# Performance work log

Measured on AMD Instinct MI355X. Metric: run time of the kernel, lower is better.

Reference implementation:

```python
import jax, jax.numpy as jnp
import numpy as np

NS, L, H = 8, 2048, 1024
M, E, K = 4096, 8, 2
EPS = 1e-9

def setup_inputs() -> dict:
    key = jax.random.key(0)
    ks = jax.random.split(key, 5)
    s = 0.02
    return {
        "x": jax.random.normal(ks[0], (NS, L, H), jnp.float32),
        "Wr": jax.random.normal(ks[1], (H, E), jnp.float32) * s,
        "br": jnp.zeros((E,), jnp.float32),
        "W1": jax.random.normal(ks[2], (E, H, M), jnp.float32) * s,
        "b1": jnp.zeros((E, M), jnp.float32),
        "W2": jax.random.normal(ks[3], (E, M, H), jnp.float32) * s,
        "b2": jnp.zeros((E, H), jnp.float32),
    }

def reference(x, Wr, br, W1, b1, W2, b2):
    ns, seq, h = x.shape
    flat = x.reshape(-1, h)                      # (N, H); grouping only reshapes, math is per-token
    logits = flat @ Wr + br                      # (N, E)
    probs = jax.nn.softmax(logits, axis=-1)
    vals, idx = jax.lax.top_k(probs, K)          # (N, K)
    w = vals / (jnp.sum(vals, axis=-1, keepdims=True) + EPS)
    out_acc = jnp.zeros_like(flat)
    weight_acc = jnp.zeros((flat.shape[0],), flat.dtype)
    for e in range(E):                           # fixed small expert loop
        we = jnp.sum(w * (idx == e), axis=-1)    # (N,) combine weight for expert e
        hmid = jax.nn.gelu(flat @ W1[e] + b1[e], approximate=False)
        y = hmid @ W2[e] + b2[e]
        out_acc = out_acc + we[:, None] * y
        weight_acc = weight_acc + we
    out = out_acc / (weight_acc[:, None] + EPS)
    return out.reshape(ns, seq, h)
```

## Files before the change

### kernel.cpp

```cpp
#include <hip/hip_runtime.h>
#include <hip/hip_bf16.h>
#include <math.h>

#define NTOK 16384
#define HDIM 1024
#define MDIM 4096
#define NEXP 8
#define EPSV 1e-9f
#define RTOK 32

typedef unsigned short u16;
typedef __attribute__((ext_vector_type(4))) float f32x4;
typedef __attribute__((ext_vector_type(8))) __bf16 bf16x8;
typedef __attribute__((ext_vector_type(8))) unsigned short u16x8;
typedef __attribute__((ext_vector_type(4))) unsigned short u16x4;

#define ASYNC_COPY16(gptr, lptr) \
    __builtin_amdgcn_global_load_lds( \
        (const __attribute__((address_space(1))) void*)(gptr), \
        (__attribute__((address_space(3))) void*)(lptr), 16, 0, 0)

static __device__ __forceinline__ u16 f2bf(float f) {
    unsigned int u = __builtin_bit_cast(unsigned int, f);
    u += 0x7fff + ((u >> 16) & 1);
    return (u16)(u >> 16);
}

static __device__ __forceinline__ float gelu_f(float v) {
    float z2 = -1.5957691216f * v * (1.f + 0.044715f * v * v);
    return v / (1.f + __expf(z2));
}

__global__ __launch_bounds__(256) void router_kernel(
    const float* __restrict__ x, const float* __restrict__ Wr,
    const float* __restrict__ br,
    int* __restrict__ counts, int* __restrict__ ltok, float* __restrict__ lcf,
    u16* __restrict__ xb)
{
    __shared__ int   lcount[NEXP];
    __shared__ int   lbase[NEXP];
    __shared__ int   ltokL[NEXP][RTOK];
    __shared__ float lcfL[NEXP][RTOK];

    int t = threadIdx.x;
    if (t < NEXP) lcount[t] = 0;
    __syncthreads();

    int wave = t >> 6, lane = t & 63;

    for (int it = 0; it < RTOK / 4; ++it) {
        int tok = blockIdx.x * RTOK + it * 4 + wave;
        const float* xr = x + (size_t)tok * HDIM + lane * 16;

        f32x4 xv[4];
        #pragma unroll
        for (int q = 0; q < 4; q++) xv[q] = *reinterpret_cast<const f32x4*>(xr + q * 4);

        u16x8 ob0, ob1;
        #pragma unroll
        for (int j = 0; j < 4; j++) {
            ob0[j]     = f2bf(xv[0][j]);
            ob0[4 + j] = f2bf(xv[1][j]);
            ob1[j]     = f2bf(xv[2][j]);
            ob1[4 + j] = f2bf(xv[3][j]);
        }
        u16* xo = xb + (size_t)tok * HDIM + lane * 16;
        *reinterpret_cast<u16x8*>(xo)     = ob0;
        *reinterpret_cast<u16x8*>(xo + 8) = ob1;

        f32x4 acc0 = {0.f, 0.f, 0.f, 0.f};
        f32x4 acc1 = {0.f, 0.f, 0.f, 0.f};
        #pragma unroll
        for (int q = 0; q < 4; q++) {
            #pragma unroll
            for (int j = 0; j < 4; j++) {
                int h = lane * 16 + q * 4 + j;
                const float* wrow = Wr + (size_t)h * NEXP;
                f32x4 w0 = *reinterpret_cast<const f32x4*>(wrow);
                f32x4 w1 = *reinterpret_cast<const f32x4*>(wrow + 4);
                acc0 += xv[q][j] * w0;
                acc1 += xv[q][j] * w1;
            }
        }
        float a[NEXP];
        #pragma unroll
        for (int e = 0; e < 4; e++) { a[e] = acc0[e]; a[4 + e] = acc1[e]; }
        #pragma unroll
        for (int e = 0; e < NEXP; e++) {
            #pragma unroll
            for (int s = 1; s < 64; s <<= 1) a[e] += __shfl_xor(a[e], s, 64);
        }
        if (lane == 0) {
            float l[NEXP], m = -1e30f;
            #pragma unroll
            for (int e = 0; e < NEXP; e++) { l[e] = a[e] + br[e]; m = fmaxf(m, l[e]); }
            float p[NEXP], s = 0.f;
            #pragma unroll
            for (int e = 0; e < NEXP; e++) { p[e] = expf(l[e] - m); s += p[e]; }
            int i0 = 0; float v0 = p[0];
            #pragma unroll
            for (int e = 1; e < NEXP; e++) if (p[e] > v0) { v0 = p[e]; i0 = e; }
            int i1 = -1; float v1 = -1.f;
            #pragma unroll
            for (int e = 0; e < NEXP; e++) if (e != i0 && p[e] > v1) { v1 = p[e]; i1 = e; }
            v0 /= s; v1 /= s;
            float sw = v0 + v1;
            float w0 = v0 / (sw + EPSV), w1 = v1 / (sw + EPSV);
            float wa = w0 + w1;
            float c0 = w0 / (wa + EPSV), c1 = w1 / (wa + EPSV);
            int q0 = atomicAdd(&lcount[i0], 1);
            ltokL[i0][q0] = tok; lcfL[i0][q0] = c0;
            int q1 = atomicAdd(&lcount[i1], 1);
            ltokL[i1][q1] = tok; lcfL[i1][q1] = c1;
        }
    }
    __syncthreads();
    if (t < NEXP) lbase[t] = atomicAdd(&counts[t], lcount[t]);
    __syncthreads();
    #pragma unroll
    for (int e = 0; e < NEXP; e++) {
        int n = lcount[e], b = lbase[e];
        for (int j = t; j < n; j += 256) {
            ltok[e * NTOK + b + j] = ltokL[e][j];
            lcf[e * NTOK + b + j]  = lcfL[e][j];
        }
    }
}

__global__ void bases_kernel(const int* __restrict__ counts, int* __restrict__ bases)
{
    if (threadIdx.x == 0) {
        int acc = 0;
        #pragma unroll
        for (int e = 0; e < NEXP; e++) { bases[e] = acc; acc += counts[e]; }
    }
}

__global__ __launch_bounds__(256) void transpose_cvt_kernel(
    const float* __restrict__ in, u16* __restrict__ out, int R, int C)
{
    __shared__ float tile[32][33];
    const float* ine = in + (size_t)blockIdx.z * R * C;
    u16* oute = out + (size_t)blockIdx.z * R * C;
    int r0 = blockIdx.y * 32, c0 = blockIdx.x * 32;
    int t = threadIdx.x;
    int r = t >> 3, cq = t & 7;
    f32x4 v = *reinterpret_cast<const f32x4*>(ine + (size_t)(r0 + r) * C + c0 + cq * 4);
    #pragma unroll
    for (int j = 0; j < 4; j++) tile[r][cq * 4 + j] = v[j];
    __syncthreads();
    int c = t >> 3, rq = t & 7;
    u16x4 o;
    #pragma unroll
    for (int j = 0; j < 4; j++) o[j] = f2bf(tile[rq * 4 + j][c]);
    *reinterpret_cast<u16x4*>(oute + (size_t)(c0 + c) * R + r0 + rq * 4) = o;
}

template<int EPI, int GX, int GY>
__global__ __launch_bounds__(256) void gemm_kernel(
    const u16* __restrict__ A,
    const u16* __restrict__ BT_all,
    const float* __restrict__ bias_all,
    const int* __restrict__ counts,
    const int* __restrict__ bases,
    const int* __restrict__ ltok,
    const float* __restrict__ lcf,
    u16* __restrict__ hmid,
    float* __restrict__ out,
    int K, int P, int Astride, int eStart)
{
    int gz = gridDim.z;
    int nwg = GX * GY * gz;
    int orig = blockIdx.x + GX * (blockIdx.y + GY * blockIdx.z);
    int qq = nwg >> 3, rr = nwg & 7;
    int xcd = orig & 7, sub = orig >> 3;
    int wgid = (xcd < rr ? xcd * (qq + 1) : rr * (qq + 1) + (xcd - rr) * qq) + sub;
    int bx = wgid & (GX - 1);
    int rem = wgid / GX;
    int by = rem & (GY - 1);
    int bz = rem / GY;

    int e = eStart + bz;
    int nrows = counts[e];
    int row0 = by * 128;
    if (row0 >= nrows) return;
    int p0 = bx * 128;
    int slotbase = bases[e];
    const u16*   BT   = BT_all + (size_t)e * P * K;
    const float* bias = bias_all + (size_t)e * P;
    const int*   lte  = ltok + (size_t)e * NTOK;
    const float* lcfe = lcf  + (size_t)e * NTOK;

    __shared__ u16 As[128][64];
    __shared__ u16 Bs[128][64];

    int t = threadIdx.x;
    int wv = t >> 6, lane = t & 63;
    int lrow8 = lane >> 3;
    int lcol8 = lane & 7;
    int schunk = lcol8 ^ lrow8;

    const u16* aptr[4];
    const u16* bptr[4];
    #pragma unroll
    for (int i = 0; i < 4; i++) {
        int pos  = row0 + wv * 32 + i * 8 + lrow8;
        int posc = min(pos, nrows - 1);
        int arow = (EPI == 0) ? lte[posc] : (slotbase + posc);
        aptr[i] = A + (size_t)arow * Astride + schunk * 8;
        int prow = p0 + wv * 32 + i * 8 + lrow8;
        bptr[i] = BT + (size_t)prow * K + schunk * 8;
    }

    int wr = (wv >> 1) * 64, wc = (wv & 1) * 64;
    int lr = lane & 15, lg = lane >> 4;
    int lr7 = lr & 7;

    f32x4 acc[4][4];
    #pragma unroll
    for (int m = 0; m < 4; m++)
        #pragma unroll
        for (int nn = 0; nn < 4; nn++) acc[m][nn] = (f32x4){0.f, 0.f, 0.f, 0.f};

    for (int k0 = 0; k0 < K; k0 += 64) {
        #pragma unroll
        for (int i = 0; i < 4; i++) {
            ASYNC_COPY16(aptr[i] + k0, &As[wv * 32 + i * 8][0]);
            ASYNC_COPY16(bptr[i] + k0, &Bs[wv * 32 + i * 8][0]);
        }
        __syncthreads();
        #pragma unroll
        for (int kk = 0; kk < 64; kk += 32) {
            int q = kk >> 3;
            bf16x8 af[4], bf[4];
            #pragma unroll
            for (int m = 0; m < 4; m++)
                af[m] = *reinterpret_cast<const bf16x8*>(
                    &As[wr + m * 16 + lr][((q + lg) ^ lr7) * 8]);
            #pragma unroll
            for (int nn = 0; nn < 4; nn++)
                bf[nn] = *reinterpret_cast<const bf16x8*>(
                    &Bs[wc + nn * 16 + lr][((q + lg) ^ lr7) * 8]);
            #pragma unroll
            for (int m = 0; m < 4; m++)
                #pragma unroll
                for (int nn = 0; nn < 4; nn++)
                    acc[m][nn] = __builtin_amdgcn_mfma_f32_16x16x32_bf16(
                        af[m], bf[nn], acc[m][nn], 0, 0, 0);
        }
        __syncthreads();
    }

    if (EPI == 0) {
        #pragma unroll
        for (int m = 0; m < 4; m++) {
            #pragma unroll
            for (int r2 = 0; r2 < 4; r2++) {
                int pos = row0 + wr + m * 16 + lg * 4 + r2;
                if (pos < nrows) {
                    size_t ho = (size_t)(slotbase + pos) * MDIM;
                    #pragma unroll
                    for (int nn = 0; nn < 4; nn++) {
                        int col = p0 + wc + nn * 16 + lr;
                        float v = acc[m][nn][r2] + bias[col];
                        hmid[ho + col] = f2bf(gelu_f(v));
                    }
                }
            }
        }
    } else {
        #pragma unroll
        for (int m = 0; m < 4; m++) {
            #pragma unroll
            for (int r2 = 0; r2 < 4; r2++) {
                int pos = row0 + wr + m * 16 + lg * 4 + r2;
                if (pos < nrows) {
                    int tokr = lte[pos];
                    float cf = lcfe[pos];
                    float* orow = out + (size_t)tokr * HDIM;
                    #pragma unroll
                    for (int nn = 0; nn < 4; nn++) {
                        int col = p0 + wc + nn * 16 + lr;
                        float v = (acc[m][nn][r2] + bias[col]) * cf;
                        atomicAdd(orow + col, v);
                    }
                }
            }
        }
    }
}

extern "C" void kernel_launch(void* const* d_in, const int* in_sizes, int n_in,
                              void* d_out, int out_size, void* d_ws, size_t ws_size,
                              hipStream_t stream)
{
    const float* x  = (const float*)d_in[0];
    const float* Wr = (const float*)d_in[1];
    const float* br = (const float*)d_in[2];
    const float* W1 = (const float*)d_in[3];
    const float* b1 = (const float*)d_in[4];
    const float* W2 = (const float*)d_in[5];
    const float* b2 = (const float*)d_in[6];
    float* out = (float*)d_out;

    char* ws = (char*)d_ws;
    size_t off = 0;
    auto alloc = [&](size_t bytes) {
        void* p = ws + off;
        off = (off + bytes + 255) & ~(size_t)255;
        return p;
    };
    int*   counts = (int*)  alloc(NEXP * 4);
    int*   bases  = (int*)  alloc(NEXP * 4);
    int*   ltok   = (int*)  alloc((size_t)NEXP * NTOK * 4);
    float* lcf    = (float*)alloc((size_t)NEXP * NTOK * 4);
    u16*   xb     = (u16*)  alloc((size_t)NTOK * HDIM * 2);
    u16*   w1t    = (u16*)  alloc((size_t)NEXP * MDIM * HDIM * 2);
    u16*   w2t    = (u16*)  alloc((size_t)NEXP * HDIM * MDIM * 2);
    size_t fixed_end = off;
    bool grouped = (ws_size >= fixed_end + (size_t)2 * NTOK * MDIM * 2);
    u16* hmid = (u16*)alloc((grouped ? (size_t)2 * NTOK : (size_t)NTOK) * MDIM * 2);

    hipMemsetAsync(counts, 0, NEXP * 4, stream);
    hipMemsetAsync(d_out, 0, (size_t)out_size * sizeof(float), stream);

    transpose_cvt_kernel<<<dim3(MDIM / 32, HDIM / 32, NEXP), 256, 0, stream>>>(W1, w1t, HDIM, MDIM);
    transpose_cvt_kernel<<<dim3(HDIM / 32, MDIM / 32, NEXP), 256, 0, stream>>>(W2, w2t, MDIM, HDIM);
    router_kernel<<<NTOK / RTOK, 256, 0, stream>>>(x, Wr, br, counts, ltok, lcf, xb);

    if (grouped) {
        bases_kernel<<<1, 64, 0, stream>>>(counts, bases);
        gemm_kernel<0, MDIM / 128, NTOK / 128>
            <<<dim3(MDIM / 128, NTOK / 128, NEXP), 256, 0, stream>>>(
            xb, w1t, b1, counts, bases, ltok, lcf, hmid, nullptr,
            HDIM, MDIM, HDIM, 0);
        gemm_kernel<1, HDIM / 128, NTOK / 128>
            <<<dim3(HDIM / 128, NTOK / 128, NEXP), 256, 0, stream>>>(
            hmid, w2t, b2, counts, bases, ltok, lcf, nullptr, out,
            MDIM, HDIM, MDIM, 0);
    } else {
        hipMemsetAsync(bases, 0, NEXP * 4, stream);
        for (int e = 0; e < NEXP; e++) {
            gemm_kernel<0, MDIM / 128, NTOK / 128>
                <<<dim3(MDIM / 128, NTOK / 128, 1), 256, 0, stream>>>(
                xb, w1t, b1, counts, bases, ltok, lcf, hmid, nullptr,
                HDIM, MDIM, HDIM, e);
            gemm_kernel<1, HDIM / 128, NTOK / 128>
                <<<dim3(HDIM / 128, NTOK / 128, 1), 256, 0, stream>>>(
                hmid, w2t, b2, counts, bases, ltok, lcf, nullptr, out,
                MDIM, HDIM, MDIM, e);
        }
    }
}
```

Measured before the change: 991.4 us.

## Add 256x256-tile, 512-thread double-buffered GEMM for the second expert projection

Replaces the 128x128 down-projection GEMM with a new kernel that uses 256x256 output tiles, 8 waves, double-buffered LDS split into halves, and interleaved async global-to-LDS staging with MFMA phases under priority raising. Larger tiles raise arithmetic intensity and cut redundant loads of hmid and W2, and the interleaved schedule is meant to hide load latency. The cost is more LDS and registers per block, fewer blocks for small experts, and more padding waste when expert token counts are not multiples of 256.

After: 1.133 ms. +14.3%, slower.

```diff
diff --git a/kernel.cpp b/kernel.cpp
--- a/kernel.cpp
+++ b/kernel.cpp
@@ -158,15 +158,11 @@
 
 template<int EPI, int GX, int GY>
 __global__ __launch_bounds__(256) void gemm_kernel(
-    const u16* __restrict__ A,
-    const u16* __restrict__ BT_all,
+    const u16* __restrict__ A, const u16* __restrict__ BT_all,
     const float* __restrict__ bias_all,
-    const int* __restrict__ counts,
-    const int* __restrict__ bases,
-    const int* __restrict__ ltok,
-    const float* __restrict__ lcf,
-    u16* __restrict__ hmid,
-    float* __restrict__ out,
+    const int* __restrict__ counts, const int* __restrict__ bases,
+    const int* __restrict__ ltok, const float* __restrict__ lcf,
+    u16* __restrict__ hmid, float* __restrict__ out,
     int K, int P, int Astride, int eStart)
 {
     int gz = gridDim.z;
@@ -196,8 +192,7 @@
 
     int t = threadIdx.x;
     int wv = t >> 6, lane = t & 63;
-    int lrow8 = lane >> 3;
-    int lcol8 = lane & 7;
+    int lrow8 = lane >> 3, lcol8 = lane & 7;
     int schunk = lcol8 ^ lrow8;
 
     const u16* aptr[4];
@@ -288,6 +283,167 @@
             }
         }
     }
+}
+
+template<int GX, int GY>
+__global__ __launch_bounds__(512, 2) void gemm2_kernel(
+    const u16* __restrict__ A,
+    const u16* __restrict__ BT_all,
+    const float* __restrict__ bias_all,
+    const int* __restrict__ counts,
+    const int* __restrict__ bases,
+    const int* __restrict__ ltok,
+    const float* __restrict__ lcf,
+    float* __restrict__ out)
+{
+    constexpr int K = MDIM;
+    int gz = gridDim.z;
+    int nwg = GX * GY * gz;
+    int orig = blockIdx.x + GX * (blockIdx.y + GY * blockIdx.z);
+    int qq = nwg >> 3, rr = nwg & 7;
+    int xcd = orig & 7, sub = orig >> 3;
+    int wgid = (xcd < rr ? xcd * (qq + 1) : rr * (qq + 1) + (xcd - rr) * qq) + sub;
+    int bx = wgid & (GX - 1);
+    int rem = wgid / GX;
+    int by = rem & (GY - 1);
+    int bz = rem / GY;
+
+    int e = bz;
+    int nrows = counts[e];
+    int row0 = by * 256;
+    if (row0 >= nrows) return;
+    int p0 = bx * 256;
+    int slotbase = bases[e];
+    const u16*   BT   = BT_all + (size_t)e * HDIM * K;
+    const float* bias = bias_all + (size_t)e * HDIM;
+    const int*   lte  = ltok + (size_t)e * NTOK;
+    const float* lcfe = lcf  + (size_t)e * NTOK;
+
+    __shared__ u16 As[2][2][128][64];
+    __shared__ u16 Bs[2][2][128][64];
+
+    int t = threadIdx.x;
+    int wid = t >> 6, lane = t & 63;
+    int wm = wid >> 2;
+    int wn = wid & 3;
+    int lr = lane & 15, lg = lane >> 4;
+    int lr7 = lr & 7;
+
+    int rl = t >> 3, ch = t & 7;
+    int sc = ch ^ (rl & 7);
+    const u16* aS[2][2];
+    #pragma unroll
+    for (int i = 0; i < 2; i++)
+        #pragma unroll
+        for (int h = 0; h < 2; h++) {
+            int pos = min(row0 + i * 128 + h * 64 + rl, nrows - 1);
+            aS[i][h] = A + (size_t)(slotbase + pos) * K + sc * 8;
+        }
+    const u16* bS[2][2];
+    #pragma unroll
+    for (int i = 0; i < 2; i++)
+        #pragma unroll
+        for (int h = 0; h < 2; h++) {
+            int g = i * 2 + (rl >> 5);
+            int prow = p0 + g * 64 + h * 32 + (rl & 31);
+            bS[i][h] = BT + (size_t)prow * K + sc * 8;
+        }
+
+    f32x4 acc[8][4];
+    #pragma unroll
+    for (int m = 0; m < 8; m++)
+        #pragma unroll
+        for (int nn = 0; nn < 4; nn++) acc[m][nn] = (f32x4){0.f, 0.f, 0.f, 0.f};
+
+#define STAGE_A2(b, h, tau) do { size_t _k = (size_t)(tau) * 64; \
+    _Pragma("unroll") for (int _i = 0; _i < 2; _i++) \
+        ASYNC_COPY16(aS[_i][h] + _k, &As[b][h][_i * 64 + wid * 8][0]); } while (0)
+#define STAGE_B2(b, h, tau) do { size_t _k = (size_t)(tau) * 64; \
+    _Pragma("unroll") for (int _i = 0; _i < 2; _i++) \
+        ASYNC_COPY16(bS[_i][h] + _k, &Bs[b][h][_i * 64 + wid * 8][0]); } while (0)
+#define CH2(kk) ((((kk) * 4 + lg) ^ lr7) * 8)
+#define RD_A(h) do { _Pragma("unroll") for (int _kk = 0; _kk < 2; _kk++) \
+    _Pragma("unroll") for (int _i = 0; _i < 4; _i++) \
+        afr[_kk][_i] = *reinterpret_cast<const bf16x8*>( \
+            &As[b][h][wm * 64 + _i * 16 + lr][CH2(_kk)]); } while (0)
+#define RD_B(dst, h) do { _Pragma("unroll") for (int _kk = 0; _kk < 2; _kk++) \
+    _Pragma("unroll") for (int _j = 0; _j < 2; _j++) \
+        dst[_kk][_j] = *reinterpret_cast<const bf16x8*>( \
+            &Bs[b][h][wn * 32 + _j * 16 + lr][CH2(_kk)]); } while (0)
+#define MM(mb, bsrc, nb) do { __builtin_amdgcn_s_setprio(1); \
+    _Pragma("unroll") for (int _kk = 0; _kk < 2; _kk++) \
+    _Pragma("unroll") for (int _i = 0; _i < 4; _i++) \
+    _Pragma("unroll") for (int _j = 0; _j < 2; _j++) \
+        acc[(mb) + _i][(nb) + _j] = __builtin_amdgcn_mfma_f32_16x16x32_bf16( \
+            afr[_kk][_i], bsrc[_kk][_j], acc[(mb) + _i][(nb) + _j], 0, 0, 0); \
+    __builtin_amdgcn_s_setprio(0); } while (0)
+#define BAR2() __builtin_amdgcn_s_barrier()
+#define LGKM0() asm volatile("s_waitcnt lgkmcnt(0)" ::: "memory")
+
+    int nk = K >> 6;
+    STAGE_A2(0, 0, 0); STAGE_B2(0, 0, 0); STAGE_B2(0, 1, 0); STAGE_A2(0, 1, 0);
+    if (nk > 1) { STAGE_A2(1, 0, 1); STAGE_B2(1, 0, 1); STAGE_B2(1, 1, 1); }
+    if (nk > 2) asm volatile("s_waitcnt vmcnt(6)" ::: "memory");
+    else        asm volatile("s_waitcnt vmcnt(0)" ::: "memory");
+    BAR2();
+
+    for (int tau = 0; tau < nk; ++tau) {
+        int b = tau & 1;
+        bf16x8 afr[2][4], bA[2][2], bB[2][2];
+
+        RD_A(0);
+        RD_B(bA, 0);
+        if (tau + 1 < nk) STAGE_A2(b ^ 1, 1, tau + 1);
+        BAR2(); LGKM0();
+        MM(0, bA, 0);
+        BAR2();
+
+        RD_B(bB, 1);
+        if (tau + 2 < nk) STAGE_A2(b, 0, tau + 2);
+        BAR2(); LGKM0();
+        MM(0, bB, 2);
+        BAR2();
+
+        RD_A(1);
+        if (tau + 2 < nk) STAGE_B2(b, 0, tau + 2);
+        BAR2(); LGKM0();
+        MM(4, bB, 2);
+        BAR2();
+
+        if (tau + 2 < nk) STAGE_B2(b, 1, tau + 2);
+        BAR2();
+        MM(4, bA, 0);
+        if (tau + 2 < nk) asm volatile("s_waitcnt vmcnt(6)" ::: "memory");
+        else              asm volatile("s_waitcnt vmcnt(0)" ::: "memory");
+        BAR2();
+    }
+
+    #pragma unroll
+    for (int m = 0; m < 8; m++) {
+        #pragma unroll
+        for (int r2 = 0; r2 < 4; r2++) {
+            int pos = row0 + wm * 128 + (m >> 2) * 64 + (m & 3) * 16 + lg * 4 + r2;
+            if (pos < nrows) {
+                int tokr = lte[pos];
+                float cf = lcfe[pos];
+                float* orow = out + (size_t)tokr * HDIM;
+                #pragma unroll
+                for (int nn = 0; nn < 4; nn++) {
+                    int col = p0 + wn * 64 + (nn >> 1) * 32 + (nn & 1) * 16 + lr;
+                    float v = (acc[m][nn][r2] + bias[col]) * cf;
+                    atomicAdd(orow + col, v);
+                }
+            }
+        }
+    }
+#undef STAGE_A2
+#undef STAGE_B2
+#undef CH2
+#undef RD_A
+#undef RD_B
+#undef MM
+#undef BAR2
+#undef LGKM0
 }
 
 extern "C" void kernel_launch(void* const* d_in, const int* in_sizes, int n_in,
@@ -334,10 +490,9 @@
             <<<dim3(MDIM / 128, NTOK / 128, NEXP), 256, 0, stream>>>(
             xb, w1t, b1, counts, bases, ltok, lcf, hmid, nullptr,
             HDIM, MDIM, HDIM, 0);
-        gemm_kernel<1, HDIM / 128, NTOK / 128>
-            <<<dim3(HDIM / 128, NTOK / 128, NEXP), 256, 0, stream>>>(
-            hmid, w2t, b2, counts, bases, ltok, lcf, nullptr, out,
-            MDIM, HDIM, MDIM, 0);
+        gemm2_kernel<HDIM / 256, NTOK / 256>
+            <<<dim3(HDIM / 256, NTOK / 256, NEXP), 512, 0, stream>>>(
+            hmid, w2t, b2, counts, bases, ltok, lcf, out);
     } else {
         hipMemsetAsync(bases, 0, NEXP * 4, stream);
         for (int e = 0; e < NEXP; e++) {
```
